# Kernel tuning notes

Hardware: AMD Instinct MI355X
Metric: run time of the kernel (lower is better)

## Reference

```python
import jax, jax.numpy as jnp
import numpy as np

EMBED_DIM = 1024
NUM_HEADS = 16
HEAD_DIM = EMBED_DIM // NUM_HEADS


def setup_inputs() -> dict:
    key = jax.random.key(0)
    k_x, k_wqkv, k_bqkv, k_wout, k_bout = jax.random.split(key, 5)
    s = 1.0 / np.sqrt(EMBED_DIM)
    return {
        "x": jax.random.normal(k_x, (2, 2048, EMBED_DIM), dtype=jnp.float32),
        "w_qkv": jax.random.uniform(k_wqkv, (EMBED_DIM, 3 * EMBED_DIM), jnp.float32, -s, s),
        "b_qkv": jax.random.uniform(k_bqkv, (3 * EMBED_DIM,), jnp.float32, -s, s),
        "w_out": jax.random.uniform(k_wout, (EMBED_DIM, EMBED_DIM), jnp.float32, -s, s),
        "b_out": jax.random.uniform(k_bout, (EMBED_DIM,), jnp.float32, -s, s),
    }


def reference(x, w_qkv, b_qkv, w_out, b_out):
    B, S, D = x.shape
    H, Hd = NUM_HEADS, HEAD_DIM
    # qkv projection, then per-head chunk: layout matches torch view(B,S,H,3*Hd).chunk(3,-1)
    qkv = (x @ w_qkv + b_qkv).reshape(B, S, H, 3, Hd)  # [B,S,H,3,Hd]
    q = qkv[..., 0, :]  # [B,S,H,Hd]
    k = qkv[..., 1, :]
    v = qkv[..., 2, :]
    scale = 1.0 / np.sqrt(Hd).astype(np.float32)
    scores = jnp.einsum("bqhd,bkhd->bhqk", q, k) * scale  # [B,H,S,S]
    probs = jax.nn.softmax(scores, axis=-1)
    out = jnp.einsum("bhqk,bkhd->bqhd", probs, v).reshape(B, S, D)
    return out @ w_out + b_out
```

## Files before the change

kernel.cpp:

```cpp
#include <hip/hip_runtime.h>
#include <hip/hip_bf16.h>


typedef __bf16 bf16;
typedef __bf16 bf16x8 __attribute__((ext_vector_type(8)));
typedef float  f32x4  __attribute__((ext_vector_type(4)));
typedef float  f32x16 __attribute__((ext_vector_type(16)));
typedef unsigned int uint;
typedef unsigned int uint2v __attribute__((ext_vector_type(2)));

__device__ __forceinline__ void gload_lds16(const void* g, void* l) {
  __builtin_amdgcn_global_load_lds(
      (const __attribute__((address_space(1))) unsigned int*)g,
      (__attribute__((address_space(3))) unsigned int*)l, 16, 0, 0);
}

__device__ __forceinline__ uint pkbf16(float lo, float hi) {
  union { bf16 h[2]; uint u; } t;
  t.h[0] = (bf16)lo; t.h[1] = (bf16)hi;
  return t.u;
}

__device__ __forceinline__ void pl32swapu(uint& a, uint& b) {
  uint2v r = __builtin_amdgcn_permlane32_swap(a, b, false, false);
  a = r.x; b = r.y;
}
__device__ __forceinline__ void pl32swapf(float& a, float& b) {
  uint ua = __builtin_bit_cast(uint, a), ub = __builtin_bit_cast(uint, b);
  pl32swapu(ua, ub);
  a = __builtin_bit_cast(float, ua); b = __builtin_bit_cast(float, ub);
}

__global__ __launch_bounds__(256) void k_convert(const float* __restrict__ in,
                                                 bf16* __restrict__ out, int n) {
  int i = (blockIdx.x * blockDim.x + threadIdx.x) * 8;
  if (i >= n) return;
  float4 a = *(const float4*)(in + i);
  float4 b = *(const float4*)(in + i + 4);
  bf16x8 o;
  o[0] = (bf16)a.x; o[1] = (bf16)a.y; o[2] = (bf16)a.z; o[3] = (bf16)a.w;
  o[4] = (bf16)b.x; o[5] = (bf16)b.y; o[6] = (bf16)b.z; o[7] = (bf16)b.w;
  *(bf16x8*)(out + i) = o;
}

template<bool PERM>
__global__ __launch_bounds__(256) void k_transpose(const float* __restrict__ in,
                                                   bf16* __restrict__ out, int K, int N) {
  __shared__ float tile[32][33];
  int n0 = blockIdx.x * 32, k0 = blockIdx.y * 32;
  int tx = threadIdx.x, ty = threadIdx.y;
#pragma unroll
  for (int i = 0; i < 4; i++)
    tile[ty + i * 8][tx] = in[(size_t)(k0 + ty + i * 8) * N + n0 + tx];
  __syncthreads();
#pragma unroll
  for (int i = 0; i < 4; i++) {
    int n = n0 + ty + i * 8;
    int row = n;
    if (PERM) {
      int rem = n % 192;
      row = (rem >> 6) * 1024 + (n / 192) * 64 + (rem & 63);
    }
    out[(size_t)row * K + k0 + tx] = (bf16)tile[tx][ty + i * 8];
  }
}

template<int BM, int BN>
__device__ __forceinline__ void gemm_tile(const bf16* __restrict__ A, const bf16* __restrict__ B,
                                          int K, int m0, int n0,
                                          bf16* As, bf16* Bs, f32x4 acc[BM / 32][BN / 32]) {
  const int tid  = threadIdx.x;
  const int lane = tid & 63;
  const int wr   = (tid >> 7) & 1;
  const int wc   = (tid >> 6) & 1;
  auto stage = [&](int k0, int b) {
#pragma unroll
    for (int i = 0; i < BM / 64; i++) {
      int row = i * 64 + (tid >> 2);
      int sw  = (tid & 3) ^ (row & 3);
      gload_lds16(A + (size_t)(m0 + row) * K + k0 + sw * 8, (char*)As + b * (BM * 64) + i * 4096 + tid * 16);
    }
#pragma unroll
    for (int i = 0; i < BN / 64; i++) {
      int row = i * 64 + (tid >> 2);
      int sw  = (tid & 3) ^ (row & 3);
      gload_lds16(B + (size_t)(n0 + row) * K + k0 + sw * 8, (char*)Bs + b * (BN * 64) + i * 4096 + tid * 16);
    }
  };
  stage(0, 0);
  const int nk = K / 32;
  for (int t = 0; t < nk; t++) {
    const int cur = t & 1;
    if (t + 1 < nk) {
      stage((t + 1) * 32, cur ^ 1);
      if constexpr (BM / 64 + BN / 64 == 4) asm volatile("s_waitcnt vmcnt(4)" ::: "memory");
      else                                  asm volatile("s_waitcnt vmcnt(3)" ::: "memory");
    } else {
      asm volatile("s_waitcnt vmcnt(0)" ::: "memory");
    }
    __builtin_amdgcn_s_barrier();
    asm volatile("" ::: "memory");
    bf16x8 af[BM / 32], bfr[BN / 32];
#pragma unroll
    for (int r = 0; r < BM / 32; r++) {
      int ra = wr * (BM / 2) + r * 16 + (lane & 15);
      af[r]  = *(const bf16x8*)((const char*)As + cur * (BM * 64) + ra * 64 + ((((lane >> 4) << 4)) ^ ((ra & 3) << 4)));
    }
#pragma unroll
    for (int c = 0; c < BN / 32; c++) {
      int rb = wc * (BN / 2) + c * 16 + (lane & 15);
      bfr[c] = *(const bf16x8*)((const char*)Bs + cur * (BN * 64) + rb * 64 + ((((lane >> 4) << 4)) ^ ((rb & 3) << 4)));
    }
#pragma unroll
    for (int r = 0; r < BM / 32; r++)
#pragma unroll
      for (int c = 0; c < BN / 32; c++)
        acc[r][c] = __builtin_amdgcn_mfma_f32_16x16x32_bf16(af[r], bfr[c], acc[r][c], 0, 0, 0);
    asm volatile("" ::: "memory");
    __builtin_amdgcn_s_barrier();
    asm volatile("" ::: "memory");
  }
}

__global__ __launch_bounds__(256) void k_gemm_qkv(const bf16* __restrict__ A, const bf16* __restrict__ Bt,
                                                  const float* __restrict__ bias,
                                                  bf16* __restrict__ qb, bf16* __restrict__ kb,
                                                  bf16* __restrict__ vtb) {
  __shared__ char GS[32768];
  bf16* As = (bf16*)GS;
  bf16* Bs = (bf16*)(GS + 16384);
  int m0 = blockIdx.x * 128, n0 = blockIdx.y * 128;
  f32x4 zero = {0.f, 0.f, 0.f, 0.f};
  f32x4 acc[4][4];
#pragma unroll
  for (int r = 0; r < 4; r++)
#pragma unroll
    for (int c = 0; c < 4; c++) acc[r][c] = zero;
  gemm_tile<128, 128>(A, Bt, 1024, m0, n0, As, Bs, acc);

  const int tid  = threadIdx.x;
  const int lane = tid & 63;
  const int wr = (tid >> 7) & 1, wc = (tid >> 6) & 1;
  const int group = n0 >> 10;
  const int hb = (n0 & 1023) >> 6;
  const int b_ = m0 >> 11;
  const float QSs = 0.125f * 1.4426950408889634f;

  __syncthreads();
  char* TL = GS;
#pragma unroll
  for (int r = 0; r < 4; r++) {
    int mloc = wr * 64 + r * 16 + ((lane >> 4) << 2);
#pragma unroll
    for (int c = 0; c < 4; c++) {
      int nloc = wc * 64 + c * 16 + (lane & 15);
      int np = n0 + nloc;
      float bv = bias[((np & 1023) >> 6) * 192 + group * 64 + (np & 63)];
#pragma unroll
      for (int g = 0; g < 4; g++) {
        float v = acc[r][c][g] + bv;
        if (group == 0) v *= QSs;
        int row = (group < 2) ? (mloc + g) : nloc;
        int col = (group < 2) ? nloc : (mloc + g);
        *(bf16*)(TL + row * 256 + col * 2) = (bf16)v;
      }
    }
  }
  __syncthreads();
  if (group < 2) {
    bf16* dst = (group == 0) ? qb : kb;
#pragma unroll
    for (int it = 0; it < 8; it++) {
      int cid = it * 256 + tid;
      int sl = cid >> 4, sub = cid & 15;
      int hh = hb + (sub >> 3), ck = sub & 7;
      bf16x8 v8 = *(const bf16x8*)(TL + sl * 256 + (sub << 4));
      *(bf16x8*)(dst + ((size_t)(b_ * 16 + hh) * 2048 + (m0 & 2047) + sl) * 64 + ck * 8) = v8;
    }
  } else {
#pragma unroll
    for (int it = 0; it < 8; it++) {
      int cid = it * 256 + tid;
      int row = cid >> 4, ck = cid & 15;
      int hh = hb + (row >> 6), dd = row & 63;
      bf16x8 v8 = *(const bf16x8*)(TL + row * 256 + (ck << 4));
      *(bf16x8*)(vtb + ((size_t)(b_ * 16 + hh) * 64 + dd) * 2048 + (m0 & 2047) + ck * 8) = v8;
    }
  }
}

__global__ __launch_bounds__(256) void k_gemm_out(const bf16* __restrict__ A, const bf16* __restrict__ Bt,
                                                  const float* __restrict__ bias,
                                                  float* __restrict__ out) {
  __shared__ bf16 As[2 * 64 * 32];
  __shared__ bf16 Bs[2 * 128 * 32];
  int m0 = blockIdx.x * 64, n0 = blockIdx.y * 128;
  f32x4 zero = {0.f, 0.f, 0.f, 0.f};
  f32x4 acc[2][4];
#pragma unroll
  for (int r = 0; r < 2; r++)
#pragma unroll
    for (int c = 0; c < 4; c++) acc[r][c] = zero;
  gemm_tile<64, 128>(A, Bt, 1024, m0, n0, As, Bs, acc);
  const int lane = threadIdx.x & 63;
  const int wr = (threadIdx.x >> 7) & 1, wc = (threadIdx.x >> 6) & 1;
#pragma unroll
  for (int r = 0; r < 2; r++) {
    int mbase = m0 + wr * 32 + r * 16 + ((lane >> 4) << 2);
#pragma unroll
    for (int c = 0; c < 4; c++) {
      int n = n0 + wc * 64 + c * 16 + (lane & 15);
      float bv = bias[n];
#pragma unroll
      for (int g = 0; g < 4; g++)
        out[(size_t)(mbase + g) * 1024 + n] = acc[r][c][g] + bv;
    }
  }
}

__global__ __launch_bounds__(512, 4) void k_attn(const bf16* __restrict__ qb, const bf16* __restrict__ kb,
                                                 const bf16* __restrict__ vtb, bf16* __restrict__ ob) {
  __shared__ char SMEM[65536];
  const int tid  = threadIdx.x;
  const int lane = tid & 63;
  const int wave = tid >> 6;
  const int qsub = wave & 3;
  const int half = wave >> 2;
  const int ln31 = lane & 31;
  const int g    = lane >> 5;

  int l = blockIdx.x;
  int x = l & 7, j = l >> 3;
  int qt = j & 15;
  int bh = x * 4 + (j >> 4);

  const int q0 = qt * 128 + qsub * 32;

  bf16x8 qf[4];
  {
    const bf16* qp = qb + ((size_t)bh * 2048 + q0 + ln31) * 64 + g * 8;
#pragma unroll
    for (int dc = 0; dc < 4; dc++) qf[dc] = *(const bf16x8*)(qp + dc * 16);
  }

  const f32x16 z16 = 0.f;
  f32x16 O0 = 0.f, O1 = 0.f;
  float lacc[4] = {0.f, 0.f, 0.f, 0.f};
  bf16x8 pf[4];

  const int r0 = tid >> 3, c0 = tid & 7;
  const int swb = (c0 ^ (r0 & 7)) * 8;
  const bf16* kg0 = kb  + ((size_t)bh * 2048 +        r0) * 64 + swb;
  const bf16* kg1 = kb  + ((size_t)bh * 2048 + 1024 + r0) * 64 + swb;
  const bf16* vg0 = vtb + ((size_t)bh * 64 + r0) * 2048 +        swb;
  const bf16* vg1 = vtb + ((size_t)bh * 64 + r0) * 2048 + 1024 + swb;
  auto stage = [&](int t, int s) {
    char* base = SMEM + s * 32768 + tid * 16;
    gload_lds16(kg0 + (size_t)t * 4096, base);
    gload_lds16(kg1 + (size_t)t * 4096, base + 8192);
    gload_lds16(vg0 + t * 64,           base + 16384);
    gload_lds16(vg1 + t * 64,           base + 24576);
  };

  const int rs = (ln31 & 7) << 4;

  auto qk = [&](const char* Kc, f32x16& s0v, f32x16& s1v) {
    const char* kr0 = Kc + ln31 * 128;
    const char* kr1 = Kc + (32 + ln31) * 128;
    {
      bf16x8 k0 = *(const bf16x8*)(kr0 + ((g << 4) ^ rs));
      bf16x8 k1 = *(const bf16x8*)(kr1 + ((g << 4) ^ rs));
      s0v = __builtin_amdgcn_mfma_f32_32x32x16_bf16(k0, qf[0], z16, 0, 0, 0);
      s1v = __builtin_amdgcn_mfma_f32_32x32x16_bf16(k1, qf[0], z16, 0, 0, 0);
    }
#pragma unroll
    for (int dc = 1; dc < 4; dc++) {
      bf16x8 ka = *(const bf16x8*)(kr0 + (((dc * 2 + g) << 4) ^ rs));
      bf16x8 kb_ = *(const bf16x8*)(kr1 + (((dc * 2 + g) << 4) ^ rs));
      s0v = __builtin_amdgcn_mfma_f32_32x32x16_bf16(ka, qf[dc], s0v, 0, 0, 0);
      s1v = __builtin_amdgcn_mfma_f32_32x32x16_bf16(kb_, qf[dc], s1v, 0, 0, 0);
    }
  };

  auto pv = [&](const char* Vc) {
#pragma unroll
    for (int kc = 0; kc < 4; kc++) {
      bf16x8 vf0 = *(const bf16x8*)(Vc + ln31 * 128 + (((kc * 2 + g) << 4) ^ rs));
      bf16x8 vf1 = *(const bf16x8*)(Vc + (32 + ln31) * 128 + (((kc * 2 + g) << 4) ^ rs));
      O0 = __builtin_amdgcn_mfma_f32_32x32x16_bf16(vf0, pf[kc], O0, 0, 0, 0);
      O1 = __builtin_amdgcn_mfma_f32_32x32x16_bf16(vf1, pf[kc], O1, 0, 0, 0);
    }
  };

  auto softmax = [&](f32x16& s0v, f32x16& s1v) {
#pragma unroll
    for (int r = 0; r < 16; r++) {
      s0v[r] = __builtin_amdgcn_exp2f(s0v[r]);
      s1v[r] = __builtin_amdgcn_exp2f(s1v[r]);
    }
#pragma unroll
    for (int r = 0; r < 4; r++)
      lacc[r] += ((s0v[r] + s0v[r + 4]) + (s0v[r + 8] + s0v[r + 12]))
               + ((s1v[r] + s1v[r + 4]) + (s1v[r + 8] + s1v[r + 12]));
#pragma unroll
    for (int kc = 0; kc < 4; kc++) {
      const int rb = (kc & 1) * 8;
      uint w0, w1, w2, w3;
      if (kc < 2) {
        w0 = pkbf16(s0v[rb + 0], s0v[rb + 1]); w1 = pkbf16(s0v[rb + 2], s0v[rb + 3]);
        w2 = pkbf16(s0v[rb + 4], s0v[rb + 5]); w3 = pkbf16(s0v[rb + 6], s0v[rb + 7]);
      } else {
        w0 = pkbf16(s1v[rb + 0], s1v[rb + 1]); w1 = pkbf16(s1v[rb + 2], s1v[rb + 3]);
        w2 = pkbf16(s1v[rb + 4], s1v[rb + 5]); w3 = pkbf16(s1v[rb + 6], s1v[rb + 7]);
      }
      pl32swapu(w0, w2);
      pl32swapu(w1, w3);
      union { uint w[4]; bf16x8 v; } pu;
      pu.w[0] = w0; pu.w[1] = w1; pu.w[2] = w2; pu.w[3] = w3;
      pf[kc] = pu.v;
    }
  };

  stage(0, 0);
  asm volatile("s_waitcnt vmcnt(0)" ::: "memory");
  __builtin_amdgcn_s_barrier();
  asm volatile("" ::: "memory");
  stage(1, 1);
  f32x16 sA, sB;
  qk(SMEM + half * 8192, sA, sB);
  softmax(sA, sB);

  for (int t = 1; t < 16; t++) {
    asm volatile("s_waitcnt vmcnt(0)" ::: "memory");
    __builtin_amdgcn_s_barrier();
    asm volatile("" ::: "memory");
    const char* Kc = SMEM + (t & 1) * 32768 + half * 8192;
    const char* Vp = SMEM + ((t - 1) & 1) * 32768 + (2 + half) * 8192;
    __builtin_amdgcn_s_setprio(1);
    qk(Kc, sA, sB);
    pv(Vp);
    __builtin_amdgcn_s_setprio(0);
    asm volatile("" ::: "memory");
    __builtin_amdgcn_s_barrier();
    asm volatile("" ::: "memory");
    if (t + 1 < 16) stage(t + 1, (t + 1) & 1);
    softmax(sA, sB);
    asm volatile("" ::: "memory");
  }
  pv(SMEM + 32768 + (2 + half) * 8192);

  float l_r = (lacc[0] + lacc[1]) + (lacc[2] + lacc[3]);
  { float o = l_r; pl32swapf(l_r, o); l_r += o; }

  float* Opart = (float*)SMEM;
  float* Ls    = (float*)(SMEM + 36864);
  __syncthreads();
  if (half == 1) {
    float* my = Opart + (qsub * 64 + lane) * 36;
#pragma unroll
    for (int c = 0; c < 4; c++) {
      f32x4 a = {O0[c * 4], O0[c * 4 + 1], O0[c * 4 + 2], O0[c * 4 + 3]};
      f32x4 b = {O1[c * 4], O1[c * 4 + 1], O1[c * 4 + 2], O1[c * 4 + 3]};
      *(f32x4*)(my + c * 4) = a;
      *(f32x4*)(my + 16 + c * 4) = b;
    }
    if (lane < 32) Ls[qsub * 32 + ln31] = l_r;
  }
  __syncthreads();
  bf16 (*Os)[32][72] = reinterpret_cast<bf16 (*)[32][72]>(SMEM + 40960);
  if (half == 0) {
    const float* pr = Opart + (qsub * 64 + lane) * 36;
#pragma unroll
    for (int c = 0; c < 4; c++) {
      f32x4 a = *(const f32x4*)(pr + c * 4);
      f32x4 b = *(const f32x4*)(pr + 16 + c * 4);
#pragma unroll
      for (int k = 0; k < 4; k++) { O0[c * 4 + k] += a[k]; O1[c * 4 + k] += b[k]; }
    }
    l_r += Ls[qsub * 32 + ln31];
    float inv = 1.0f / l_r;
#pragma unroll
    for (int r = 0; r < 16; r++) {
      int d0 = (r & 3) + 8 * (r >> 2) + 4 * g;
      Os[qsub][ln31][d0]      = (bf16)(O0[r] * inv);
      Os[qsub][ln31][d0 + 32] = (bf16)(O1[r] * inv);
    }
  }
  __syncthreads();
  if (half == 0) {
    int b_ = bh >> 4, h = bh & 15;
#pragma unroll
    for (int it = 0; it < 4; it++) {
      int cid = it * 64 + lane;
      int row = cid >> 3, c = cid & 7;
      bf16x8 v8o = *(const bf16x8*)&Os[qsub][row][c * 8];
      *(bf16x8*)(ob + ((size_t)(b_ * 2048 + q0 + row)) * 1024 + h * 64 + c * 8) = v8o;
    }
  }
}

extern "C" void kernel_launch(void* const* d_in, const int* in_sizes, int n_in,
                              void* d_out, int out_size, void* d_ws, size_t ws_size,
                              hipStream_t stream) {
  const float* x     = (const float*)d_in[0];
  const float* w_qkv = (const float*)d_in[1];
  const float* b_qkv = (const float*)d_in[2];
  const float* w_out = (const float*)d_in[3];
  const float* b_out = (const float*)d_in[4];
  float* out = (float*)d_out;

  char* ws = (char*)d_ws;
  bf16* xb  = (bf16*)ws;
  bf16* wqT = (bf16*)(ws + (8ull  << 20));
  bf16* woT = (bf16*)(ws + (14ull << 20));
  bf16* qb  = (bf16*)(ws + (16ull << 20));
  bf16* kb  = (bf16*)(ws + (24ull << 20));
  bf16* vtb = (bf16*)(ws + (32ull << 20));

  k_convert<<<2048, 256, 0, stream>>>(x, xb, 4194304);
  k_transpose<true><<<dim3(96, 32), dim3(32, 8), 0, stream>>>(w_qkv, wqT, 1024, 3072);
  k_transpose<false><<<dim3(32, 32), dim3(32, 8), 0, stream>>>(w_out, woT, 1024, 1024);
  k_gemm_qkv<<<dim3(32, 24), 256, 0, stream>>>(xb, wqT, b_qkv, qb, kb, vtb);
  k_attn<<<512, 512, 0, stream>>>(qb, kb, vtb, xb);
  k_gemm_out<<<dim3(64, 8), 256, 0, stream>>>(xb, woT, b_out, out);
}
```

Baseline: 123.7 us.

## Deepen GEMM pipeline to four stages and pad attention LDS layout

The GEMM main loop moves from a two-stage to a four-stage LDS ring with three tiles in flight, and drops the trailing barrier per iteration. This doubles LDS use in both GEMM kernels. The attention kernel swaps the XOR-swizzled K/V layout for a padded 144-byte row stride, loaded via 9-chunk-per-row indexing with wave 0 issuing extra loads. It also drops the software pipelining that overlapped the PV of the previous tile with the QK of the current one, running QK, softmax and PV sequentially per tile. The bigger LDS footprint may cut occupancy, and losing the QK/PV overlap can expose latency.

```diff
diff --git a/kernel.cpp b/kernel.cpp
--- a/kernel.cpp
+++ b/kernel.cpp
@@ -73,33 +73,37 @@
   const int lane = tid & 63;
   const int wr   = (tid >> 7) & 1;
   const int wc   = (tid >> 6) & 1;
+  constexpr int LA = BM / 64, LB = BN / 64;
   auto stage = [&](int k0, int b) {
 #pragma unroll
-    for (int i = 0; i < BM / 64; i++) {
+    for (int i = 0; i < LA; i++) {
       int row = i * 64 + (tid >> 2);
       int sw  = (tid & 3) ^ (row & 3);
       gload_lds16(A + (size_t)(m0 + row) * K + k0 + sw * 8, (char*)As + b * (BM * 64) + i * 4096 + tid * 16);
     }
 #pragma unroll
-    for (int i = 0; i < BN / 64; i++) {
+    for (int i = 0; i < LB; i++) {
       int row = i * 64 + (tid >> 2);
       int sw  = (tid & 3) ^ (row & 3);
       gload_lds16(B + (size_t)(n0 + row) * K + k0 + sw * 8, (char*)Bs + b * (BN * 64) + i * 4096 + tid * 16);
     }
   };
-  stage(0, 0);
   const int nk = K / 32;
+  stage(0, 0); stage(32, 1); stage(64, 2);
   for (int t = 0; t < nk; t++) {
-    const int cur = t & 1;
-    if (t + 1 < nk) {
-      stage((t + 1) * 32, cur ^ 1);
-      if constexpr (BM / 64 + BN / 64 == 4) asm volatile("s_waitcnt vmcnt(4)" ::: "memory");
-      else                                  asm volatile("s_waitcnt vmcnt(3)" ::: "memory");
+    if (t < nk - 2) {
+      if constexpr (LA + LB == 4) asm volatile("s_waitcnt vmcnt(8)" ::: "memory");
+      else                        asm volatile("s_waitcnt vmcnt(6)" ::: "memory");
+    } else if (t < nk - 1) {
+      if constexpr (LA + LB == 4) asm volatile("s_waitcnt vmcnt(4)" ::: "memory");
+      else                        asm volatile("s_waitcnt vmcnt(3)" ::: "memory");
     } else {
       asm volatile("s_waitcnt vmcnt(0)" ::: "memory");
     }
     __builtin_amdgcn_s_barrier();
     asm volatile("" ::: "memory");
+    if (t + 3 < nk) stage((t + 3) * 32, (t + 3) & 3);
+    const int cur = t & 3;
     bf16x8 af[BM / 32], bfr[BN / 32];
 #pragma unroll
     for (int r = 0; r < BM / 32; r++) {
@@ -116,8 +120,6 @@
 #pragma unroll
       for (int c = 0; c < BN / 32; c++)
         acc[r][c] = __builtin_amdgcn_mfma_f32_16x16x32_bf16(af[r], bfr[c], acc[r][c], 0, 0, 0);
-    asm volatile("" ::: "memory");
-    __builtin_amdgcn_s_barrier();
     asm volatile("" ::: "memory");
   }
 }
@@ -126,9 +128,9 @@
                                                   const float* __restrict__ bias,
                                                   bf16* __restrict__ qb, bf16* __restrict__ kb,
                                                   bf16* __restrict__ vtb) {
-  __shared__ char GS[32768];
+  __shared__ char GS[65536];
   bf16* As = (bf16*)GS;
-  bf16* Bs = (bf16*)(GS + 16384);
+  bf16* Bs = (bf16*)(GS + 32768);
   int m0 = blockIdx.x * 128, n0 = blockIdx.y * 128;
   f32x4 zero = {0.f, 0.f, 0.f, 0.f};
   f32x4 acc[4][4];
@@ -192,8 +194,8 @@
 __global__ __launch_bounds__(256) void k_gemm_out(const bf16* __restrict__ A, const bf16* __restrict__ Bt,
                                                   const float* __restrict__ bias,
                                                   float* __restrict__ out) {
-  __shared__ bf16 As[2 * 64 * 32];
-  __shared__ bf16 Bs[2 * 128 * 32];
+  __shared__ bf16 As[4 * 64 * 32];
+  __shared__ bf16 Bs[4 * 128 * 32];
   int m0 = blockIdx.x * 64, n0 = blockIdx.y * 128;
   f32x4 zero = {0.f, 0.f, 0.f, 0.f};
   f32x4 acc[2][4];
@@ -220,7 +222,7 @@
 
 __global__ __launch_bounds__(512, 4) void k_attn(const bf16* __restrict__ qb, const bf16* __restrict__ kb,
                                                  const bf16* __restrict__ vtb, bf16* __restrict__ ob) {
-  __shared__ char SMEM[65536];
+  __shared__ char SMEM[73728];
   const int tid  = threadIdx.x;
   const int lane = tid & 63;
   const int wave = tid >> 6;
@@ -248,51 +250,61 @@
   float lacc[4] = {0.f, 0.f, 0.f, 0.f};
   bf16x8 pf[4];
 
-  const int r0 = tid >> 3, c0 = tid & 7;
-  const int swb = (c0 ^ (r0 & 7)) * 8;
-  const bf16* kg0 = kb  + ((size_t)bh * 2048 +        r0) * 64 + swb;
-  const bf16* kg1 = kb  + ((size_t)bh * 2048 + 1024 + r0) * 64 + swb;
-  const bf16* vg0 = vtb + ((size_t)bh * 64 + r0) * 2048 +        swb;
-  const bf16* vg1 = vtb + ((size_t)bh * 64 + r0) * 2048 + 1024 + swb;
+  const int c1 = tid, r1 = c1 / 9, cc1 = c1 % 9;
+  const int of1 = (cc1 == 8 ? 0 : cc1) * 8;
+  const int c2 = 512 + tid, r2 = c2 / 9, cc2 = c2 % 9;
+  const int of2 = (cc2 == 8 ? 0 : cc2) * 8;
+  const bf16* kg0a = kb  + ((size_t)bh * 2048 +        r1) * 64 + of1;
+  const bf16* kg1a = kb  + ((size_t)bh * 2048 + 1024 + r1) * 64 + of1;
+  const bf16* vg0a = vtb + ((size_t)bh * 64 + r1) * 2048 +        of1;
+  const bf16* vg1a = vtb + ((size_t)bh * 64 + r1) * 2048 + 1024 + of1;
+  const bf16* kg0b = kb  + ((size_t)bh * 2048 +        r2) * 64 + of2;
+  const bf16* kg1b = kb  + ((size_t)bh * 2048 + 1024 + r2) * 64 + of2;
+  const bf16* vg0b = vtb + ((size_t)bh * 64 + r2) * 2048 +        of2;
+  const bf16* vg1b = vtb + ((size_t)bh * 64 + r2) * 2048 + 1024 + of2;
   auto stage = [&](int t, int s) {
-    char* base = SMEM + s * 32768 + tid * 16;
-    gload_lds16(kg0 + (size_t)t * 4096, base);
-    gload_lds16(kg1 + (size_t)t * 4096, base + 8192);
-    gload_lds16(vg0 + t * 64,           base + 16384);
-    gload_lds16(vg1 + t * 64,           base + 24576);
+    char* bs = SMEM + s * 36864;
+    gload_lds16(kg0a + (size_t)t * 4096, bs +         c1 * 16);
+    gload_lds16(kg1a + (size_t)t * 4096, bs + 9216  + c1 * 16);
+    gload_lds16(vg0a + t * 64,           bs + 18432 + c1 * 16);
+    gload_lds16(vg1a + t * 64,           bs + 27648 + c1 * 16);
+    if (wave == 0) {
+      gload_lds16(kg0b + (size_t)t * 4096, bs +         c2 * 16);
+      gload_lds16(kg1b + (size_t)t * 4096, bs + 9216  + c2 * 16);
+      gload_lds16(vg0b + t * 64,           bs + 18432 + c2 * 16);
+      gload_lds16(vg1b + t * 64,           bs + 27648 + c2 * 16);
+    }
   };
 
-  const int rs = (ln31 & 7) << 4;
-
-  auto qk = [&](const char* Kc, f32x16& s0v, f32x16& s1v) {
-    const char* kr0 = Kc + ln31 * 128;
-    const char* kr1 = Kc + (32 + ln31) * 128;
+  stage(0, 0);
+  for (int t = 0; t < 16; t++) {
+    asm volatile("s_waitcnt vmcnt(0)" ::: "memory");
+    __builtin_amdgcn_s_barrier();
+    asm volatile("" ::: "memory");
+    if (t + 1 < 16) stage(t + 1, (t + 1) & 1);
+
+    const char* Kc = SMEM + (t & 1) * 36864 + half * 9216;
+    const char* Vc = SMEM + (t & 1) * 36864 + 18432 + half * 9216;
+    const char* kr0 = Kc + ln31 * 144;
+    const char* kr1 = Kc + (32 + ln31) * 144;
+
+    f32x16 s0v, s1v;
+    __builtin_amdgcn_s_setprio(1);
     {
-      bf16x8 k0 = *(const bf16x8*)(kr0 + ((g << 4) ^ rs));
-      bf16x8 k1 = *(const bf16x8*)(kr1 + ((g << 4) ^ rs));
+      bf16x8 k0 = *(const bf16x8*)(kr0 + (g << 4));
+      bf16x8 k1 = *(const bf16x8*)(kr1 + (g << 4));
       s0v = __builtin_amdgcn_mfma_f32_32x32x16_bf16(k0, qf[0], z16, 0, 0, 0);
       s1v = __builtin_amdgcn_mfma_f32_32x32x16_bf16(k1, qf[0], z16, 0, 0, 0);
     }
 #pragma unroll
     for (int dc = 1; dc < 4; dc++) {
-      bf16x8 ka = *(const bf16x8*)(kr0 + (((dc * 2 + g) << 4) ^ rs));
-      bf16x8 kb_ = *(const bf16x8*)(kr1 + (((dc * 2 + g) << 4) ^ rs));
+      bf16x8 ka = *(const bf16x8*)(kr0 + ((dc * 2 + g) << 4));
+      bf16x8 kb_ = *(const bf16x8*)(kr1 + ((dc * 2 + g) << 4));
       s0v = __builtin_amdgcn_mfma_f32_32x32x16_bf16(ka, qf[dc], s0v, 0, 0, 0);
       s1v = __builtin_amdgcn_mfma_f32_32x32x16_bf16(kb_, qf[dc], s1v, 0, 0, 0);
     }
-  };
-
-  auto pv = [&](const char* Vc) {
-#pragma unroll
-    for (int kc = 0; kc < 4; kc++) {
-      bf16x8 vf0 = *(const bf16x8*)(Vc + ln31 * 128 + (((kc * 2 + g) << 4) ^ rs));
-      bf16x8 vf1 = *(const bf16x8*)(Vc + (32 + ln31) * 128 + (((kc * 2 + g) << 4) ^ rs));
-      O0 = __builtin_amdgcn_mfma_f32_32x32x16_bf16(vf0, pf[kc], O0, 0, 0, 0);
-      O1 = __builtin_amdgcn_mfma_f32_32x32x16_bf16(vf1, pf[kc], O1, 0, 0, 0);
-    }
-  };
-
-  auto softmax = [&](f32x16& s0v, f32x16& s1v) {
+    __builtin_amdgcn_s_setprio(0);
+
 #pragma unroll
     for (int r = 0; r < 16; r++) {
       s0v[r] = __builtin_amdgcn_exp2f(s0v[r]);
@@ -319,35 +331,18 @@
       pu.w[0] = w0; pu.w[1] = w1; pu.w[2] = w2; pu.w[3] = w3;
       pf[kc] = pu.v;
     }
-  };
-
-  stage(0, 0);
-  asm volatile("s_waitcnt vmcnt(0)" ::: "memory");
-  __builtin_amdgcn_s_barrier();
-  asm volatile("" ::: "memory");
-  stage(1, 1);
-  f32x16 sA, sB;
-  qk(SMEM + half * 8192, sA, sB);
-  softmax(sA, sB);
-
-  for (int t = 1; t < 16; t++) {
-    asm volatile("s_waitcnt vmcnt(0)" ::: "memory");
-    __builtin_amdgcn_s_barrier();
-    asm volatile("" ::: "memory");
-    const char* Kc = SMEM + (t & 1) * 32768 + half * 8192;
-    const char* Vp = SMEM + ((t - 1) & 1) * 32768 + (2 + half) * 8192;
+
     __builtin_amdgcn_s_setprio(1);
-    qk(Kc, sA, sB);
-    pv(Vp);
+#pragma unroll
+    for (int kc = 0; kc < 4; kc++) {
+      bf16x8 vf0 = *(const bf16x8*)(Vc + ln31 * 144 + ((kc * 2 + g) << 4));
+      bf16x8 vf1 = *(const bf16x8*)(Vc + (32 + ln31) * 144 + ((kc * 2 + g) << 4));
+      O0 = __builtin_amdgcn_mfma_f32_32x32x16_bf16(vf0, pf[kc], O0, 0, 0, 0);
+      O1 = __builtin_amdgcn_mfma_f32_32x32x16_bf16(vf1, pf[kc], O1, 0, 0, 0);
+    }
     __builtin_amdgcn_s_setprio(0);
     asm volatile("" ::: "memory");
-    __builtin_amdgcn_s_barrier();
-    asm volatile("" ::: "memory");
-    if (t + 1 < 16) stage(t + 1, (t + 1) & 1);
-    softmax(sA, sB);
-    asm volatile("" ::: "memory");
-  }
-  pv(SMEM + 32768 + (2 + half) * 8192);
+  }
 
   float l_r = (lacc[0] + lacc[1]) + (lacc[2] + lacc[3]);
   { float o = l_r; pl32swapf(l_r, o); l_r += o; }
```

Measured after the change: 122.7 us. Within noise of the previous version (-0.8%).
